# Kernel tuning notes

Hardware: AMD Instinct MI355X
Metric: run time of the kernel (lower is better)

Reference implementation:

```python
import jax, jax.numpy as jnp
import numpy as np

H, W, D = 1024, 1024, 128


def setup_inputs() -> dict:
    key = jax.random.key(0)
    ks = jax.random.split(key, 7)
    x = jax.random.normal(ks[0], (2, H, W), dtype=jnp.float32)
    s1 = 1.0 / np.sqrt(4.0)
    s2 = 1.0 / np.sqrt(float(D))
    W1 = jax.random.uniform(ks[1], (4, D), jnp.float32, -s1, s1)
    b1 = jax.random.uniform(ks[2], (D,), jnp.float32, -s1, s1)
    W2 = jax.random.uniform(ks[3], (D, D), jnp.float32, -s2, s2)
    b2 = jax.random.uniform(ks[4], (D,), jnp.float32, -s2, s2)
    W3 = jax.random.uniform(ks[5], (D, D), jnp.float32, -s2, s2)
    b3 = jax.random.uniform(ks[6], (D,), jnp.float32, -s2, s2)
    return dict(x=x, W1=W1, b1=b1, W2=W2, b2=b2, W3=W3, b3=b3)


def _masked_norm(v, mask):
    # normalize(v) = (v - min) / (max - min), min/max over nonzero pixels only
    big = jnp.float32(1e30)
    vmin = jnp.min(jnp.where(mask, v, big))
    vmax = jnp.max(jnp.where(mask, v, -big))
    return (v - vmin) / (vmax - vmin)


def reference(x, W1, b1, W2, b2, W3, b3):
    x0, x1 = x[0], x[1]                      # real, imag maps [H, W]
    mask = x0 != 0                            # nonzero-context pixels
    w = mask.astype(x.dtype).reshape(-1)      # [H*W] 0/1 weights

    rows = jnp.broadcast_to(jnp.arange(H, dtype=x.dtype)[:, None], (H, W))
    cols = jnp.broadcast_to(jnp.arange(W, dtype=x.dtype)[None, :], (H, W))
    nr = _masked_norm(rows, mask)
    nc = _masked_norm(cols, mask)

    # per-point features [H*W, 4]: (norm row, norm col, real, imag)
    feats = jnp.stack([nr, nc, x0, x1], axis=-1).reshape(-1, 4)

    # fc3(relu(fc2(fc1(.)))) — note: no activation between fc1 and fc2
    h = feats @ W1 + b1                       # [N, 128]
    h = h @ W2 + b2
    h = jax.nn.relu(h)
    out = h @ W3 + b3                         # [N, 128]

    # mean over nonzero points only
    return (w[:, None] * out).sum(0) / w.sum()
```

## Files before the change

kernel.cpp:

```cpp
#include <hip/hip_runtime.h>
#include <climits>

#define HH 1024
#define WW 1024
#define DD 128
#define NPIX (HH * WW)
#define NSB 256
#define NBB 1024

#define RMINP 1024
#define RMAXP 1280
#define CMINP 1536
#define CMAXP 1792
#define CNTP  2048
#define PART  8192

typedef __attribute__((ext_vector_type(2))) float f32x2;

__device__ __forceinline__ void d_stats(const float* __restrict__ x0, int blk,
                                        int tid, int* __restrict__ wsi,
                                        int (*sred)[8]) {
    const float4* x4 = (const float4*)(x0) + (size_t)blk * 1024;
    int any0, any1, any2, any3;
    int cmn = INT_MAX, cmx = -1, cnt = 0;
    int c4 = 4 * tid;
    {
        float4 v;
        bool z0, z1, z2, z3;
        #define STAT_K(K, ANY)                                                 \
            v = x4[K * 256 + tid];                                             \
            z0 = v.x != 0.f; z1 = v.y != 0.f; z2 = v.z != 0.f; z3 = v.w != 0.f;\
            ANY = (int)(z0 | z1 | z2 | z3);                                    \
            if (ANY) {                                                         \
                cmn = min(cmn, z0 ? c4 : (z1 ? c4+1 : (z2 ? c4+2 : c4+3)));    \
                cmx = max(cmx, z3 ? c4+3 : (z2 ? c4+2 : (z1 ? c4+1 : c4)));    \
            }                                                                  \
            cnt += (int)z0 + (int)z1 + (int)z2 + (int)z3;
        STAT_K(0, any0) STAT_K(1, any1) STAT_K(2, any2) STAT_K(3, any3)
        #undef STAT_K
    }
    for (int off = 32; off >= 1; off >>= 1) {
        cmn = min(cmn, __shfl_xor(cmn, off, 64));
        cmx = max(cmx, __shfl_xor(cmx, off, 64));
        cnt += __shfl_xor(cnt, off, 64);
        any0 |= __shfl_xor(any0, off, 64);
        any1 |= __shfl_xor(any1, off, 64);
        any2 |= __shfl_xor(any2, off, 64);
        any3 |= __shfl_xor(any3, off, 64);
    }
    int wave = tid >> 6;
    if ((tid & 63) == 0) {
        sred[wave][0] = cmn; sred[wave][1] = cmx; sred[wave][2] = cnt;
        sred[wave][3] = any0; sred[wave][4] = any1;
        sred[wave][5] = any2; sred[wave][6] = any3;
    }
    __syncthreads();
    if (tid == 0) {
        int a = sred[0][0], b = sred[0][1], c = sred[0][2];
        int f0 = sred[0][3], f1 = sred[0][4], f2 = sred[0][5], f3 = sred[0][6];
        for (int w = 1; w < 4; ++w) {
            a = min(a, sred[w][0]); b = max(b, sred[w][1]); c += sred[w][2];
            f0 |= sred[w][3]; f1 |= sred[w][4]; f2 |= sred[w][5]; f3 |= sred[w][6];
        }
        int r0 = blk * 4;
        wsi[RMINP + blk] = f0 ? r0 : (f1 ? r0+1 : (f2 ? r0+2 : (f3 ? r0+3 : INT_MAX)));
        wsi[RMAXP + blk] = f3 ? r0+3 : (f2 ? r0+2 : (f1 ? r0+1 : (f0 ? r0 : -1)));
        wsi[CMINP + blk] = a;
        wsi[CMAXP + blk] = b;
        wsi[CNTP  + blk] = c;
    }
}

__global__ __launch_bounds__(256) void kA(const float* __restrict__ x0,
                                          const float* __restrict__ W1,
                                          const float* __restrict__ b1,
                                          const float* __restrict__ W2,
                                          const float* __restrict__ b2,
                                          const float* __restrict__ b3,
                                          float* __restrict__ out,
                                          float* __restrict__ wsf,
                                          int* __restrict__ wsi) {
    __shared__ int sred[4][8];
    int blk = blockIdx.x, tid = threadIdx.x;
    if (blk < NSB) { d_stats(x0, blk, tid, wsi, sred); return; }
    if (tid < 128) {
        int j = tid;
        float p0 = 0.f, p1 = 0.f, p2 = 0.f, p3 = 0.f, cc = 0.f;
        #pragma unroll 8
        for (int d = 0; d < DD; ++d) {
            float w2 = W2[d * DD + j];
            p0 = fmaf(W1[0 * DD + d], w2, p0);
            p1 = fmaf(W1[1 * DD + d], w2, p1);
            p2 = fmaf(W1[2 * DD + d], w2, p2);
            p3 = fmaf(W1[3 * DD + d], w2, p3);
            cc = fmaf(b1[d],          w2, cc);
        }
        wsf[64 + 0 * DD + j] = p0;
        wsf[64 + 1 * DD + j] = p1;
        wsf[64 + 2 * DD + j] = p2;
        wsf[64 + 3 * DD + j] = p3;
        wsf[576 + j] = cc + b2[j];
        out[j] = b3[j];
    }
}

__global__ __launch_bounds__(256) void kB(const float* __restrict__ x0,
                                          const float* __restrict__ x1,
                                          float* __restrict__ wsf,
                                          const int* __restrict__ wsi) {
    __shared__ float sv_f[4096];
    __shared__ unsigned short lidx[1024];
    __shared__ int   lcnt;
    __shared__ int   sred[4][4];
    __shared__ float fred[128][9];

    int tid = threadIdx.x, blk = blockIdx.x;
    int wv = tid >> 6, lane = tid & 63;

    if (tid == 0) lcnt = 0;

    int rmn = wsi[RMINP + tid], rmx = wsi[RMAXP + tid];
    int cmn = wsi[CMINP + tid], cmx = wsi[CMAXP + tid];
    for (int off = 32; off >= 1; off >>= 1) {
        rmn = min(rmn, __shfl_xor(rmn, off, 64));
        rmx = max(rmx, __shfl_xor(rmx, off, 64));
        cmn = min(cmn, __shfl_xor(cmn, off, 64));
        cmx = max(cmx, __shfl_xor(cmx, off, 64));
    }
    if (lane == 0) {
        sred[wv][0] = rmn; sred[wv][1] = rmx;
        sred[wv][2] = cmn; sred[wv][3] = cmx;
    }
    __syncthreads();
    rmn = min(min(sred[0][0], sred[1][0]), min(sred[2][0], sred[3][0]));
    rmx = max(max(sred[0][1], sred[1][1]), max(sred[2][1], sred[3][1]));
    cmn = min(min(sred[0][2], sred[1][2]), min(sred[2][2], sred[3][2]));
    cmx = max(max(sred[0][3], sred[1][3]), max(sred[2][3], sred[3][3]));

    const float4* x04 = (const float4*)(x0) + (size_t)blk * 256;
    const float4* x14 = (const float4*)(x1) + (size_t)blk * 256;
    float4* sv4 = (float4*)sv_f;
    {
        float4 va = x04[tid];
        float4 vb = x14[tid];
        sv4[2 * tid]     = make_float4(va.x, va.y, vb.x, vb.y);
        sv4[2 * tid + 1] = make_float4(va.z, va.w, vb.z, vb.w);
        int p4 = 4 * tid;
        if (va.x == 0.f) { int p = atomicAdd(&lcnt, 1); lidx[p] = (unsigned short)(p4 + 0); }
        if (va.y == 0.f) { int p = atomicAdd(&lcnt, 1); lidx[p] = (unsigned short)(p4 + 1); }
        if (va.z == 0.f) { int p = atomicAdd(&lcnt, 1); lidx[p] = (unsigned short)(p4 + 2); }
        if (va.w == 0.f) { int p = atomicAdd(&lcnt, 1); lidx[p] = (unsigned short)(p4 + 3); }
    }
    __syncthreads();

    int ft = tid & 31;
    int cq = tid >> 5;
    int row = blk;
    float rs = 1.0f / (float)(rmx - rmn);
    float cs = 1.0f / (float)(cmx - cmn);

    f32x2 M2v[4], M3v[4], tv[4], st[4], acc[4];
    float a1v[4], rb[4];
    float accsub[4];
    #pragma unroll
    for (int k = 0; k < 4; ++k) {
        int f = ft + 32 * k;
        float M2 = wsf[64 + 2 * DD + f];
        float M3 = wsf[64 + 3 * DD + f];
        float a0 = wsf[64 + 0 * DD + f] * rs;
        float a1 = wsf[64 + 1 * DD + f] * cs;
        float cp = wsf[576 + f] - (float)rmn * a0 - (float)cmn * a1;
        rb[k]  = fmaf((float)row, a0, cp);
        a1v[k] = a1;
        float tA = fmaf((float)(cq * 128), a1, rb[k]);
        M2v[k] = (f32x2)M2;
        M3v[k] = (f32x2)M3;
        tv[k].x = tA; tv[k].y = tA + a1;
        st[k] = (f32x2)(a1 + a1);
        acc[k] = (f32x2)0.f;
        accsub[k] = 0.f;
    }

    const float4* p = sv4 + cq * 64;
    #pragma unroll 4
    for (int q = 0; q < 64; ++q) {
        float4 v = p[q];
        f32x2 v0; v0.x = v.x; v0.y = v.y;
        f32x2 v1; v1.x = v.z; v1.y = v.w;
        #pragma unroll
        for (int k = 0; k < 4; ++k) {
            f32x2 d = __builtin_elementwise_fma(v0, M2v[k],
                        __builtin_elementwise_fma(v1, M3v[k], tv[k]));
            f32x2 r = __builtin_elementwise_max(d, (f32x2)0.f);
            acc[k] += r;
            tv[k] += st[k];
        }
    }

    int nz = lcnt;
    for (int ii = 0; ii < nz; ++ii) {
        int px = lidx[ii];
        if ((px >> 7) == cq) {
            float v0 = sv_f[(px >> 1) * 4 + (px & 1)];
            float v1 = sv_f[(px >> 1) * 4 + 2 + (px & 1)];
            #pragma unroll
            for (int k = 0; k < 4; ++k) {
                float tp = fmaf((float)px, a1v[k], rb[k]);
                accsub[k] += fmaxf(fmaf(v0, M2v[k].x, fmaf(v1, M3v[k].x, tp)), 0.f);
            }
        }
    }

    #pragma unroll
    for (int k = 0; k < 4; ++k)
        fred[ft + 32 * k][cq] = (acc[k].x + acc[k].y) - accsub[k];
    __syncthreads();
    if (tid < 128) {
        const float* fr = fred[tid];
        float s = ((fr[0] + fr[1]) + (fr[2] + fr[3]))
                + ((fr[4] + fr[5]) + (fr[6] + fr[7]));
        wsf[PART + (size_t)tid * NBB + blk] = s;
    }
}

__global__ __launch_bounds__(256) void kC(const float* __restrict__ wsf,
                                          const int* __restrict__ wsi,
                                          const float* __restrict__ W3,
                                          float* __restrict__ out) {
    __shared__ float sred[4];
    __shared__ int   cred[4];
    __shared__ float mf_sh;
    int f = blockIdx.x, tid = threadIdx.x;
    int wv = tid >> 6, lane = tid & 63;

    int c = wsi[CNTP + tid];
    for (int off = 32; off >= 1; off >>= 1) c += __shfl_xor(c, off, 64);
    if (lane == 0) cred[wv] = c;

    const float4* p = (const float4*)(wsf + PART + (size_t)f * NBB);
    float4 v = p[tid];
    float S = (v.x + v.y) + (v.z + v.w);
    for (int off = 32; off >= 1; off >>= 1) S += __shfl_xor(S, off, 64);
    if (lane == 0) sred[wv] = S;
    __syncthreads();
    if (tid == 0) {
        float tot = (sred[0] + sred[1]) + (sred[2] + sred[3]);
        float cnt = (float)(cred[0] + cred[1] + cred[2] + cred[3]);
        mf_sh = tot / cnt;
    }
    __syncthreads();

    if (tid < 128) {
        float mf = mf_sh;
        atomicAdd(&out[tid], mf * W3[f * DD + tid]);
    }
}

extern "C" void kernel_launch(void* const* d_in, const int* in_sizes, int n_in,
                              void* d_out, int out_size, void* d_ws, size_t ws_size,
                              hipStream_t stream) {
    const float* x  = (const float*)d_in[0];
    const float* x0 = x;
    const float* x1 = x + NPIX;
    const float* W1 = (const float*)d_in[1];
    const float* b1 = (const float*)d_in[2];
    const float* W2 = (const float*)d_in[3];
    const float* b2 = (const float*)d_in[4];
    const float* W3 = (const float*)d_in[5];
    const float* b3 = (const float*)d_in[6];
    float* outp = (float*)d_out;
    float* wsf  = (float*)d_ws;
    int*   wsi  = (int*)d_ws;

    hipLaunchKernelGGL(kA, dim3(NSB + 1), dim3(256), 0, stream,
                       x0, W1, b1, W2, b2, b3, outp, wsf, wsi);
    hipLaunchKernelGGL(kB, dim3(NBB), dim3(256), 0, stream, x0, x1, wsf, wsi);
    hipLaunchKernelGGL(kC, dim3(DD), dim3(256), 0, stream, wsf, wsi, W3, outp);
}
```

Before: 31.50 us.

## Stream pixels directly from global memory and subtract masked pixels inline

kB no longer stages the row's x0/x1 pixels in LDS or builds a list of zero pixels with LDS atomics. Each wave now covers 256 columns and reads float4s straight from global memory, since all lanes of a wave read the same addresses. Each lane handles 2 features instead of 4, and a zero pixel's contribution is subtracted inline when it is found in the loop. This removes the LDS staging, the atomics, a barrier and the serial zero-pixel pass. In exchange, each wave makes redundant global loads, has fewer independent FMA chains per thread, and adds a branch inside the hot loop.

Measured after the change: 36.74 us. +16.7%, slower.

```diff
diff --git a/kernel.cpp b/kernel.cpp
--- a/kernel.cpp
+++ b/kernel.cpp
@@ -108,16 +108,11 @@
                                           const float* __restrict__ x1,
                                           float* __restrict__ wsf,
                                           const int* __restrict__ wsi) {
-    __shared__ float sv_f[4096];
-    __shared__ unsigned short lidx[1024];
-    __shared__ int   lcnt;
     __shared__ int   sred[4][4];
-    __shared__ float fred[128][9];
+    __shared__ float fred[4][132];
 
     int tid = threadIdx.x, blk = blockIdx.x;
     int wv = tid >> 6, lane = tid & 63;
-
-    if (tid == 0) lcnt = 0;
 
     int rmn = wsi[RMINP + tid], rmx = wsi[RMAXP + tid];
     int cmn = wsi[CMINP + tid], cmx = wsi[CMAXP + tid];
@@ -137,88 +132,80 @@
     cmn = min(min(sred[0][2], sred[1][2]), min(sred[2][2], sred[3][2]));
     cmx = max(max(sred[0][3], sred[1][3]), max(sred[2][3], sred[3][3]));
 
-    const float4* x04 = (const float4*)(x0) + (size_t)blk * 256;
-    const float4* x14 = (const float4*)(x1) + (size_t)blk * 256;
-    float4* sv4 = (float4*)sv_f;
-    {
-        float4 va = x04[tid];
-        float4 vb = x14[tid];
-        sv4[2 * tid]     = make_float4(va.x, va.y, vb.x, vb.y);
-        sv4[2 * tid + 1] = make_float4(va.z, va.w, vb.z, vb.w);
-        int p4 = 4 * tid;
-        if (va.x == 0.f) { int p = atomicAdd(&lcnt, 1); lidx[p] = (unsigned short)(p4 + 0); }
-        if (va.y == 0.f) { int p = atomicAdd(&lcnt, 1); lidx[p] = (unsigned short)(p4 + 1); }
-        if (va.z == 0.f) { int p = atomicAdd(&lcnt, 1); lidx[p] = (unsigned short)(p4 + 2); }
-        if (va.w == 0.f) { int p = atomicAdd(&lcnt, 1); lidx[p] = (unsigned short)(p4 + 3); }
-    }
-    __syncthreads();
-
-    int ft = tid & 31;
-    int cq = tid >> 5;
     int row = blk;
+    int colbase = wv * 256;
     float rs = 1.0f / (float)(rmx - rmn);
     float cs = 1.0f / (float)(cmx - cmn);
 
-    f32x2 M2v[4], M3v[4], tv[4], st[4], acc[4];
-    float a1v[4], rb[4];
-    float accsub[4];
+    f32x2 M2v[2], M3v[2], tAv[2], tBv[2], stv[2], accA[2], accB[2];
+    float a1s[2], rbs[2];
     #pragma unroll
-    for (int k = 0; k < 4; ++k) {
-        int f = ft + 32 * k;
+    for (int k = 0; k < 2; ++k) {
+        int f = lane + 64 * k;
         float M2 = wsf[64 + 2 * DD + f];
         float M3 = wsf[64 + 3 * DD + f];
         float a0 = wsf[64 + 0 * DD + f] * rs;
         float a1 = wsf[64 + 1 * DD + f] * cs;
         float cp = wsf[576 + f] - (float)rmn * a0 - (float)cmn * a1;
-        rb[k]  = fmaf((float)row, a0, cp);
-        a1v[k] = a1;
-        float tA = fmaf((float)(cq * 128), a1, rb[k]);
+        float rb = fmaf((float)row, a0, cp);
+        rbs[k] = rb; a1s[k] = a1;
+        float t0 = fmaf((float)colbase, a1, rb);
         M2v[k] = (f32x2)M2;
         M3v[k] = (f32x2)M3;
-        tv[k].x = tA; tv[k].y = tA + a1;
-        st[k] = (f32x2)(a1 + a1);
-        acc[k] = (f32x2)0.f;
-        accsub[k] = 0.f;
-    }
-
-    const float4* p = sv4 + cq * 64;
+        tAv[k].x = t0;            tAv[k].y = t0 + a1;
+        tBv[k].x = t0 + 2.f * a1; tBv[k].y = t0 + 3.f * a1;
+        stv[k] = (f32x2)(4.f * a1);
+        accA[k] = (f32x2)0.f; accB[k] = (f32x2)0.f;
+    }
+
+    const float4* p0 = (const float4*)(x0 + (size_t)row * WW + colbase);
+    const float4* p1 = (const float4*)(x1 + (size_t)row * WW + colbase);
+
     #pragma unroll 4
     for (int q = 0; q < 64; ++q) {
-        float4 v = p[q];
-        f32x2 v0; v0.x = v.x; v0.y = v.y;
-        f32x2 v1; v1.x = v.z; v1.y = v.w;
+        float4 v0 = p0[q];
+        float4 v1 = p1[q];
+        f32x2 v0A; v0A.x = v0.x; v0A.y = v0.y;
+        f32x2 v0B; v0B.x = v0.z; v0B.y = v0.w;
+        f32x2 v1A; v1A.x = v1.x; v1A.y = v1.y;
+        f32x2 v1B; v1B.x = v1.z; v1B.y = v1.w;
         #pragma unroll
-        for (int k = 0; k < 4; ++k) {
-            f32x2 d = __builtin_elementwise_fma(v0, M2v[k],
-                        __builtin_elementwise_fma(v1, M3v[k], tv[k]));
-            f32x2 r = __builtin_elementwise_max(d, (f32x2)0.f);
-            acc[k] += r;
-            tv[k] += st[k];
-        }
-    }
-
-    int nz = lcnt;
-    for (int ii = 0; ii < nz; ++ii) {
-        int px = lidx[ii];
-        if ((px >> 7) == cq) {
-            float v0 = sv_f[(px >> 1) * 4 + (px & 1)];
-            float v1 = sv_f[(px >> 1) * 4 + 2 + (px & 1)];
-            #pragma unroll
-            for (int k = 0; k < 4; ++k) {
-                float tp = fmaf((float)px, a1v[k], rb[k]);
-                accsub[k] += fmaxf(fmaf(v0, M2v[k].x, fmaf(v1, M3v[k].x, tp)), 0.f);
-            }
+        for (int k = 0; k < 2; ++k) {
+            f32x2 dA = __builtin_elementwise_fma(v0A, M2v[k],
+                         __builtin_elementwise_fma(v1A, M3v[k], tAv[k]));
+            f32x2 dB = __builtin_elementwise_fma(v0B, M2v[k],
+                         __builtin_elementwise_fma(v1B, M3v[k], tBv[k]));
+            accA[k] += __builtin_elementwise_max(dA, (f32x2)0.f);
+            accB[k] += __builtin_elementwise_max(dB, (f32x2)0.f);
+            tAv[k] += stv[k];
+            tBv[k] += stv[k];
+        }
+        if ((v0.x == 0.f) | (v0.y == 0.f) | (v0.z == 0.f) | (v0.w == 0.f)) {
+            int col = colbase + 4 * q;
+            #define SUBPX(VZ, V1C, CI)                                         \
+                if (VZ == 0.f) {                                               \
+                    _Pragma("unroll")                                          \
+                    for (int k = 0; k < 2; ++k) {                              \
+                        float tp = fmaf((float)(CI), a1s[k], rbs[k]);          \
+                        accA[k].x -= fmaxf(fmaf(V1C, M3v[k].x, tp), 0.f);      \
+                    }                                                          \
+                }
+            SUBPX(v0.x, v1.x, col + 0)
+            SUBPX(v0.y, v1.y, col + 1)
+            SUBPX(v0.z, v1.z, col + 2)
+            SUBPX(v0.w, v1.w, col + 3)
+            #undef SUBPX
         }
     }
 
     #pragma unroll
-    for (int k = 0; k < 4; ++k)
-        fred[ft + 32 * k][cq] = (acc[k].x + acc[k].y) - accsub[k];
+    for (int k = 0; k < 2; ++k) {
+        f32x2 s = accA[k] + accB[k];
+        fred[wv][lane + 64 * k] = s.x + s.y;
+    }
     __syncthreads();
     if (tid < 128) {
-        const float* fr = fred[tid];
-        float s = ((fr[0] + fr[1]) + (fr[2] + fr[3]))
-                + ((fr[4] + fr[5]) + (fr[6] + fr[7]));
+        float s = (fred[0][tid] + fred[1][tid]) + (fred[2][tid] + fred[3][tid]);
         wsf[PART + (size_t)tid * NBB + blk] = s;
     }
 }
```
